# Kernel optimization log

Hardware: AMD Instinct MI355X
Metric: run time of the kernel (lower is better)

The kernel has to match this reference:

```python
import jax, jax.numpy as jnp
import numpy as np

B, S, D = 1, 2048, 2048
H, KVH, HD = 32, 8, 64  # heads, kv heads, head_dim
GROUPS = H // KVH
SCALE = HD ** -0.5


def rotate_half(x):
    x1, x2 = jnp.split(x, 2, axis=-1)
    return jnp.concatenate((-x2, x1), axis=-1)


def setup_inputs() -> dict:
    key = jax.random.key(0)
    ks = jax.random.split(key, 8)
    hidden_states = jax.random.normal(ks[0], (B, S, D), dtype=jnp.float32)
    # RoPE tables: [B, S, HD]
    inv_freq = 1.0 / (10000.0 ** (jnp.arange(0, HD, 2, dtype=jnp.float32) / HD))
    t = jnp.arange(S, dtype=jnp.float32)
    freqs = jnp.outer(t, inv_freq)                      # [S, HD/2]
    emb = jnp.concatenate((freqs, freqs), axis=-1)      # [S, HD]
    cos = jnp.cos(emb)[None]                            # [1, S, HD]
    sin = jnp.sin(emb)[None]
    std = 0.02
    wq = jax.random.normal(ks[1], (H * HD, D), dtype=jnp.float32) * std
    wk = jax.random.normal(ks[2], (KVH * HD, D), dtype=jnp.float32) * std
    wv = jax.random.normal(ks[3], (KVH * HD, D), dtype=jnp.float32) * std
    wo = jax.random.normal(ks[4], (D, H * HD), dtype=jnp.float32) * std
    return {"hidden_states": hidden_states, "cos": cos, "sin": sin,
            "wq": wq, "wk": wk, "wv": wv, "wo": wo}


def reference(hidden_states, cos, sin, wq, wk, wv, wo):
    b, s, d = hidden_states.shape
    # QKV projections (nn.Linear: x @ W.T), split into heads -> [B, H, S, HD]
    q = (hidden_states @ wq.T).reshape(b, s, H, HD).transpose(0, 2, 1, 3)
    k = (hidden_states @ wk.T).reshape(b, s, KVH, HD).transpose(0, 2, 1, 3)
    v = (hidden_states @ wv.T).reshape(b, s, KVH, HD).transpose(0, 2, 1, 3)
    # RoPE (unsqueeze_dim=1)
    c = cos[:, None, :, :]
    sn = sin[:, None, :, :]
    q = q * c + rotate_half(q) * sn
    k = k * c + rotate_half(k) * sn
    # GQA: repeat kv heads to match query heads
    k = jnp.repeat(k, GROUPS, axis=1)
    v = jnp.repeat(v, GROUPS, axis=1)
    # scaled causal softmax attention
    scores = jnp.einsum('bhqd,bhkd->bhqk', q, k) * SCALE
    causal = jnp.tril(jnp.ones((s, s), dtype=bool))
    scores = jnp.where(causal, scores, jnp.finfo(scores.dtype).min)
    probs = jax.nn.softmax(scores, axis=-1)
    attn = jnp.einsum('bhqk,bhkd->bhqd', probs, v)
    attn = attn.transpose(0, 2, 1, 3).reshape(b, s, H * HD)
    return attn @ wo.T
```

## Files before the change

kernel.cpp:

```cpp
#include <hip/hip_runtime.h>
#include <stdint.h>

#define SEQ   2048
#define DMODEL 2048
#define NQH   32
#define NKVH  8
#define HDIM  64
#define QN    (NQH*HDIM)
#define KVNN  (NKVH*HDIM)

typedef __bf16 bf16x8 __attribute__((ext_vector_type(8)));
typedef float  f32x4  __attribute__((ext_vector_type(4)));
typedef unsigned short u16;

__device__ __forceinline__ u16 f2bf(float f) {
  __bf16 h = (__bf16)f;
  return __builtin_bit_cast(u16, h);
}
__device__ __forceinline__ float bf2f(u16 b) {
  return __builtin_bit_cast(float, (uint32_t)b << 16);
}
__device__ __forceinline__ float fexp2(float x) {
#if __has_builtin(__builtin_amdgcn_exp2f)
  return __builtin_amdgcn_exp2f(x);
#else
  return __expf(0.69314718056f * x);
#endif
}
__device__ __forceinline__ bool probe_is_f32(const uint32_t* p) {
  return (p[0] & 0xFFFFu) == 0u;
}

__device__ __forceinline__ void glds16(const u16* g, void* lds) {
  __builtin_amdgcn_global_load_lds(
      (const __attribute__((address_space(1))) uint32_t*)g,
      (__attribute__((address_space(3))) uint32_t*)lds, 16, 0, 0);
}
__device__ __forceinline__ void wait_vm6() { asm volatile("s_waitcnt vmcnt(6)" ::: "memory"); }
__device__ __forceinline__ void wait_vm3() { asm volatile("s_waitcnt vmcnt(3)" ::: "memory"); }
__device__ __forceinline__ void wait_vm0() { asm volatile("s_waitcnt vmcnt(0)" ::: "memory"); }
__device__ __forceinline__ void raw_barrier() { __builtin_amdgcn_s_barrier(); }
__device__ __forceinline__ void mem_pin() { asm volatile("" ::: "memory"); }

__global__ __launch_bounds__(256)
void conv_all(const void* __restrict__ X, const void* __restrict__ cosv,
              const void* __restrict__ sinv, const void* __restrict__ wq,
              const void* __restrict__ wk, const void* __restrict__ wv,
              const void* __restrict__ wo,
              u16* __restrict__ Xc, u16* __restrict__ cosc, u16* __restrict__ sinc,
              u16* __restrict__ wqc, u16* __restrict__ wkc, u16* __restrict__ wvc,
              u16* __restrict__ woc)
{
  const bool f32in = probe_is_f32((const uint32_t*)cosv);
  const long t = (long)blockIdx.x * 256 + threadIdx.x;
  const void* src; u16* dst; long off;
  if      (t < 524288L)  { src = X;    dst = Xc;   off = t; }
  else if (t < 1048576L) { src = wq;   dst = wqc;  off = t - 524288L; }
  else if (t < 1179648L) { src = wk;   dst = wkc;  off = t - 1048576L; }
  else if (t < 1310720L) { src = wv;   dst = wvc;  off = t - 1179648L; }
  else if (t < 1835008L) { src = wo;   dst = woc;  off = t - 1310720L; }
  else if (t < 1851392L) { src = cosv; dst = cosc; off = t - 1835008L; }
  else                   { src = sinv; dst = sinc; off = t - 1851392L; }
  if (f32in) {
    const float4* s = (const float4*)src;
    float4 a = s[2*off], b = s[2*off + 1];
    union { u16 h[8]; uint4 u; } o;
    o.h[0]=f2bf(a.x); o.h[1]=f2bf(a.y); o.h[2]=f2bf(a.z); o.h[3]=f2bf(a.w);
    o.h[4]=f2bf(b.x); o.h[5]=f2bf(b.y); o.h[6]=f2bf(b.z); o.h[7]=f2bf(b.w);
    *(uint4*)(dst + off*8) = o.u;
  } else {
    *(uint4*)(dst + off*8) = ((const uint4*)src)[off];
  }
}

__global__ __launch_bounds__(256, 4)
void gemm_qkv(const u16* __restrict__ A,
              const u16* __restrict__ wq, const u16* __restrict__ wk,
              const u16* __restrict__ wv,
              u16* __restrict__ Qb, u16* __restrict__ Kb, u16* __restrict__ Vb)
{
  __shared__ __align__(16) u16 As[3][64][32];
  __shared__ __align__(16) u16 Bs[3][128][32];
  const int tid  = threadIdx.x;
  const int wave = tid >> 6;
  const int lane = tid & 63;
  const int quad = lane >> 4;
  const int l16  = lane & 15;
  const int m0 = blockIdx.y * 64;
  const int n0 = blockIdx.x * 128;
  const int wm = (wave & 1) * 32;
  const int wn = (wave >> 1) * 64;
  const int K = DMODEL;
  const int lr = lane >> 2;
  const int lc = (lane & 3) * 8;

  const u16* Bbase; u16* Cbase; int Cstride, nc0;
  if (n0 < 2048)      { Bbase = wq + (size_t)n0 * K;          Cbase = Qb; Cstride = QN;   nc0 = n0; }
  else if (n0 < 2560) { Bbase = wk + (size_t)(n0 - 2048) * K; Cbase = Kb; Cstride = KVNN; nc0 = n0 - 2048; }
  else                { Bbase = wv + (size_t)(n0 - 2560) * K; Cbase = Vb; Cstride = KVNN; nc0 = n0 - 2560; }

  f32x4 acc[2][4];
  #pragma unroll
  for (int i = 0; i < 2; i++)
    #pragma unroll
    for (int j = 0; j < 4; j++)
      acc[i][j] = (f32x4){0.f, 0.f, 0.f, 0.f};

  #define STAGE_QKV(b, k0)                                                        \
    do {                                                                          \
      glds16(A + (size_t)(m0 + 16*wave + lr) * K + (k0) + lc,                     \
             (char*)&As[b][0][0] + wave*1024);                                    \
      glds16(Bbase + (size_t)(16*wave + lr) * K + (k0) + lc,                      \
             (char*)&Bs[b][0][0] + wave*1024);                                    \
      glds16(Bbase + (size_t)(64 + 16*wave + lr) * K + (k0) + lc,                 \
             (char*)&Bs[b][0][0] + (4+wave)*1024);                                \
    } while (0)

  const int NT = K / 32;
  STAGE_QKV(0, 0);
  STAGE_QKV(1, 32);
  STAGE_QKV(2, 64);
  int cur = 0;
  for (int t = 0; t < NT; ++t) {
    if      (t < NT - 2) wait_vm6();
    else if (t == NT - 2) wait_vm3();
    else                  wait_vm0();
    raw_barrier();
    mem_pin();
    bf16x8 af[2], bfr[4];
    #pragma unroll
    for (int i = 0; i < 2; i++) af[i]  = *(const bf16x8*)&As[cur][wm + i*16 + l16][quad*8];
    #pragma unroll
    for (int j = 0; j < 4; j++) bfr[j] = *(const bf16x8*)&Bs[cur][wn + j*16 + l16][quad*8];
    #pragma unroll
    for (int i = 0; i < 2; i++)
      #pragma unroll
      for (int j = 0; j < 4; j++)
        acc[i][j] = __builtin_amdgcn_mfma_f32_16x16x32_bf16(af[i], bfr[j], acc[i][j], 0, 0, 0);
    raw_barrier();
    mem_pin();
    if (t + 3 < NT) STAGE_QKV(cur, (t + 3) * 32);
    cur = (cur == 2) ? 0 : cur + 1;
  }
  #undef STAGE_QKV

  #pragma unroll
  for (int i = 0; i < 2; i++) {
    const int rb = m0 + wm + i*16 + quad*4;
    #pragma unroll
    for (int j = 0; j < 4; j++) {
      const int col = nc0 + wn + j*16 + l16;
      #pragma unroll
      for (int r = 0; r < 4; r++)
        Cbase[(size_t)(rb + r) * Cstride + col] = f2bf(acc[i][j][r]);
    }
  }
}

__global__ __launch_bounds__(256, 4)
void gemm_nt(const u16* __restrict__ A, const u16* __restrict__ B,
             void* __restrict__ C, int M, int N, int K,
             const uint32_t* outprobe)
{
  __shared__ __align__(16) u16 As[3][64][32];
  __shared__ __align__(16) u16 Bs[3][128][32];
  const int tid  = threadIdx.x;
  const int wave = tid >> 6;
  const int lane = tid & 63;
  const int quad = lane >> 4;
  const int l16  = lane & 15;
  const int m0 = blockIdx.y * 64;
  const int n0 = blockIdx.x * 128;
  const int wm = (wave & 1) * 32;
  const int wn = (wave >> 1) * 64;
  const int lr = lane >> 2;
  const int lc = (lane & 3) * 8;

  f32x4 acc[2][4];
  #pragma unroll
  for (int i = 0; i < 2; i++)
    #pragma unroll
    for (int j = 0; j < 4; j++)
      acc[i][j] = (f32x4){0.f, 0.f, 0.f, 0.f};

  #define STAGE_NT(b, k0)                                                         \
    do {                                                                          \
      glds16(A + (size_t)(m0 + 16*wave + lr) * K + (k0) + lc,                     \
             (char*)&As[b][0][0] + wave*1024);                                    \
      glds16(B + (size_t)(n0 + 16*wave + lr) * K + (k0) + lc,                     \
             (char*)&Bs[b][0][0] + wave*1024);                                    \
      glds16(B + (size_t)(n0 + 64 + 16*wave + lr) * K + (k0) + lc,                \
             (char*)&Bs[b][0][0] + (4+wave)*1024);                                \
    } while (0)

  const int NT = K / 32;
  STAGE_NT(0, 0);
  STAGE_NT(1, 32);
  STAGE_NT(2, 64);
  int cur = 0;
  for (int t = 0; t < NT; ++t) {
    if      (t < NT - 2) wait_vm6();
    else if (t == NT - 2) wait_vm3();
    else                  wait_vm0();
    raw_barrier();
    mem_pin();
    bf16x8 af[2], bfr[4];
    #pragma unroll
    for (int i = 0; i < 2; i++) af[i]  = *(const bf16x8*)&As[cur][wm + i*16 + l16][quad*8];
    #pragma unroll
    for (int j = 0; j < 4; j++) bfr[j] = *(const bf16x8*)&Bs[cur][wn + j*16 + l16][quad*8];
    #pragma unroll
    for (int i = 0; i < 2; i++)
      #pragma unroll
      for (int j = 0; j < 4; j++)
        acc[i][j] = __builtin_amdgcn_mfma_f32_16x16x32_bf16(af[i], bfr[j], acc[i][j], 0, 0, 0);
    raw_barrier();
    mem_pin();
    if (t + 3 < NT) STAGE_NT(cur, (t + 3) * 32);
    cur = (cur == 2) ? 0 : cur + 1;
  }
  #undef STAGE_NT

  const bool f32out = (outprobe != nullptr) && probe_is_f32(outprobe);
  #pragma unroll
  for (int i = 0; i < 2; i++) {
    const int rb = m0 + wm + i*16 + quad*4;
    #pragma unroll
    for (int j = 0; j < 4; j++) {
      const int col = n0 + wn + j*16 + l16;
      if (f32out) {
        float* Cf = (float*)C;
        #pragma unroll
        for (int r = 0; r < 4; r++)
          Cf[(size_t)(rb + r) * N + col] = acc[i][j][r];
      } else {
        u16* Ch = (u16*)C;
        #pragma unroll
        for (int r = 0; r < 4; r++)
          Ch[(size_t)(rb + r) * N + col] = f2bf(acc[i][j][r]);
      }
    }
  }
}

__global__ void rope_k(u16* __restrict__ Kb,
                       const u16* __restrict__ cosb, const u16* __restrict__ sinb)
{
  const int idx = blockIdx.x * 256 + threadIdx.x;
  const int s = idx >> 8;
  const int rem = idx & 255;
  u16* base = Kb + (size_t)s * KVNN + (rem >> 5) * 64;
  const int d = rem & 31;
  const float x1 = bf2f(base[d]);
  const float x2 = bf2f(base[d + 32]);
  const float c  = bf2f(cosb[s * 64 + d]);
  const float sn = bf2f(sinb[s * 64 + d]);
  base[d]      = f2bf(x1 * c - x2 * sn);
  base[d + 32] = f2bf(x2 * c + x1 * sn);
}

__global__ __launch_bounds__(256)
void vtrans(const u16* __restrict__ Vb, u16* __restrict__ Vtg)
{
  __shared__ __align__(16) u16 T[64][72];
  const int tid = threadIdx.x;
  const int hkv = blockIdx.x & 7;
  const int s0  = (blockIdx.x >> 3) * 64;
  const int r = tid >> 3;
  const int c = (tid & 7) * 8;
  *(uint4*)&T[r][c]      = *(const uint4*)(Vb + (size_t)(s0 + r)      * KVNN + hkv*64 + c);
  *(uint4*)&T[r + 32][c] = *(const uint4*)(Vb + (size_t)(s0 + r + 32) * KVNN + hkv*64 + c);
  __syncthreads();
  #pragma unroll
  for (int dd = 0; dd < 64; dd += 32) {
    const int d = (tid >> 3) + dd;
    union { u16 h[8]; uint4 u; } o;
    #pragma unroll
    for (int j = 0; j < 8; j++) o.h[j] = T[c + j][d];
    *(uint4*)(Vtg + (size_t)(hkv*64 + d) * SEQ + s0 + c) = o.u;
  }
}

#define LOG2E 1.4426950408889634f

__global__ __launch_bounds__(256, 4)
void attn_kernel(const u16* __restrict__ Qb,
                 const u16* __restrict__ Kb,
                 const u16* __restrict__ Vtg,
                 u16* __restrict__ Ob,
                 const u16* __restrict__ cosb, const u16* __restrict__ sinb)
{
  __shared__ __align__(16) u16 Ks[64][72];
  __shared__ __align__(16) u16 Vt[64][72];
  __shared__ __align__(16) u16 Ps[4][16][72];

  const int tid  = threadIdx.x;
  const int wave = tid >> 6;
  const int lane = tid & 63;
  const int quad = lane >> 4;
  const int l16  = lane & 15;
  const int h    = blockIdx.x;
  const int qt   = 31 - blockIdx.y;
  const int hkv  = h >> 2;
  const int qrow0 = qt * 64 + wave * 16;
  const int ktmax = qt + 1;
  const int myq  = qrow0 + l16;

  bf16x8 qf[2];
  {
    const int qrow = qrow0 + l16;
    const u16* qp = Qb + (size_t)qrow * QN + h*64 + quad*8;
    union { bf16x8 v; u16 h8[8]; } lo, hi, cv, sv, olo, ohi;
    lo.v = *(const bf16x8*)qp;
    hi.v = *(const bf16x8*)(qp + 32);
    cv.v = *(const bf16x8*)(cosb + qrow*64 + quad*8);
    sv.v = *(const bf16x8*)(sinb + qrow*64 + quad*8);
    #pragma unroll
    for (int j = 0; j < 8; j++) {
      const float x1 = bf2f(lo.h8[j]), x2 = bf2f(hi.h8[j]);
      const float c = bf2f(cv.h8[j]), sn = bf2f(sv.h8[j]);
      olo.h8[j] = f2bf((x1*c - x2*sn) * 0.125f);
      ohi.h8[j] = f2bf((x2*c + x1*sn) * 0.125f);
    }
    qf[0] = olo.v;
    qf[1] = ohi.v;
  }

  f32x4 oacc[4];
  #pragma unroll
  for (int nt = 0; nt < 4; nt++) oacc[nt] = (f32x4){0.f, 0.f, 0.f, 0.f};
  float m_run = -1e30f, l_run = 0.f;

  const int sr = tid >> 3;
  const int sc = (tid & 7) * 8;

  uint4 k0, k1, v0, v1;
  {
    k0 = *(const uint4*)(Kb + (size_t)(sr)      * KVNN + hkv*64 + sc);
    k1 = *(const uint4*)(Kb + (size_t)(sr + 32) * KVNN + hkv*64 + sc);
    v0 = *(const uint4*)(Vtg + (size_t)(hkv*64 + sr)      * SEQ + sc);
    v1 = *(const uint4*)(Vtg + (size_t)(hkv*64 + sr + 32) * SEQ + sc);
  }

  for (int kt = 0; kt < ktmax; kt++) {
    const int kb = kt * 64;
    const bool diag = (kt == qt);

    __syncthreads();
    *(uint4*)&Ks[sr][sc]      = k0;
    *(uint4*)&Ks[sr + 32][sc] = k1;
    *(uint4*)&Vt[sr][sc]      = v0;
    *(uint4*)&Vt[sr + 32][sc] = v1;
    __syncthreads();

    if (kt + 1 < ktmax) {
      const int kn = kb + 64;
      k0 = *(const uint4*)(Kb + (size_t)(kn + sr)      * KVNN + hkv*64 + sc);
      k1 = *(const uint4*)(Kb + (size_t)(kn + sr + 32) * KVNN + hkv*64 + sc);
      v0 = *(const uint4*)(Vtg + (size_t)(hkv*64 + sr)      * SEQ + kn + sc);
      v1 = *(const uint4*)(Vtg + (size_t)(hkv*64 + sr + 32) * SEQ + kn + sc);
    }

    f32x4 sacc[4];
    #pragma unroll
    for (int nt = 0; nt < 4; nt++) sacc[nt] = (f32x4){0.f, 0.f, 0.f, 0.f};
    #pragma unroll
    for (int ks = 0; ks < 2; ks++)
      #pragma unroll
      for (int nt = 0; nt < 4; nt++)
        if (!diag || nt <= wave) {
          bf16x8 kf = *(const bf16x8*)&Ks[nt*16 + l16][ks*32 + quad*8];
          sacc[nt] = __builtin_amdgcn_mfma_f32_16x16x32_bf16(kf, qf[ks], sacc[nt], 0, 0, 0);
        }
    #pragma unroll
    for (int nt = 0; nt < 4; nt++)
      #pragma unroll
      for (int r = 0; r < 4; r++)
        sacc[nt][r] *= LOG2E;
    if (diag) {
      #pragma unroll
      for (int nt = 0; nt < 4; nt++)
        #pragma unroll
        for (int r = 0; r < 4; r++)
          if (kb + nt*16 + quad*4 + r > myq)
            sacc[nt][r] = -1e30f;
    }
    float mx = sacc[0][0];
    #pragma unroll
    for (int nt = 0; nt < 4; nt++)
      #pragma unroll
      for (int r = 0; r < 4; r++)
        if (nt | r) mx = fmaxf(mx, sacc[nt][r]);
    mx = fmaxf(mx, __shfl_xor(mx, 16));
    mx = fmaxf(mx, __shfl_xor(mx, 32));
    const float mnew = fmaxf(m_run, mx);
    const float alpha = fexp2(m_run - mnew);
    m_run = mnew;
    float rs = 0.f;
    #pragma unroll
    for (int nt = 0; nt < 4; nt++)
      #pragma unroll
      for (int r = 0; r < 4; r++) {
        const float p = fexp2(sacc[nt][r] - mnew);
        sacc[nt][r] = p;
        rs += p;
      }
    rs += __shfl_xor(rs, 16);
    rs += __shfl_xor(rs, 32);
    l_run = l_run * alpha + rs;
    #pragma unroll
    for (int nt = 0; nt < 4; nt++) {
      union { u16 h[4]; uint2 v; } pk;
      #pragma unroll
      for (int r = 0; r < 4; r++) pk.h[r] = f2bf(sacc[nt][r]);
      *(uint2*)&Ps[wave][l16][nt*16 + quad*4] = pk.v;
    }
    #pragma unroll
    for (int nt = 0; nt < 4; nt++)
      #pragma unroll
      for (int r = 0; r < 4; r++)
        oacc[nt][r] *= alpha;
    asm volatile("" ::: "memory");
    #pragma unroll
    for (int ks = 0; ks < 2; ks++) {
      if (diag && wave < 2 && ks == 1) continue;
      bf16x8 pf = *(const bf16x8*)&Ps[wave][l16][ks*32 + quad*8];
      #pragma unroll
      for (int nt = 0; nt < 4; nt++) {
        bf16x8 vf = *(const bf16x8*)&Vt[nt*16 + l16][ks*32 + quad*8];
        oacc[nt] = __builtin_amdgcn_mfma_f32_16x16x32_bf16(vf, pf, oacc[nt], 0, 0, 0);
      }
    }
  }

  {
    const float inv = 1.0f / l_run;
    #pragma unroll
    for (int nt = 0; nt < 4; nt++) {
      union { u16 h[4]; uint2 v; } ok;
      #pragma unroll
      for (int r = 0; r < 4; r++) ok.h[r] = f2bf(oacc[nt][r] * inv);
      *(uint2*)(Ob + (size_t)myq * QN + h*64 + nt*16 + quad*4) = ok.v;
    }
  }
}

extern "C" void kernel_launch(void* const* d_in, const int* in_sizes, int n_in,
                              void* d_out, int out_size, void* d_ws, size_t ws_size,
                              hipStream_t stream) {
  const void* X    = d_in[0];
  const void* cosr = d_in[1];
  const void* sinr = d_in[2];
  const void* wq   = d_in[3];
  const void* wk   = d_in[4];
  const void* wv   = d_in[5];
  const void* wo   = d_in[6];

  char* ws = (char*)d_ws;
  const size_t MB = 1024u * 1024u;
  u16* Xc   = (u16*)(ws);
  u16* wqc  = (u16*)(ws + 8*MB);
  u16* wkc  = (u16*)(ws + 16*MB);
  u16* wvc  = (u16*)(ws + 18*MB);
  u16* woc  = (u16*)(ws + 20*MB);
  u16* cosc = (u16*)(ws + 28*MB);
  u16* sinc = (u16*)(ws + 28*MB + 256*1024);
  u16* Qb   = (u16*)(ws + 28*MB + 512*1024);
  u16* Kb   = (u16*)(ws + 36*MB + 512*1024);
  u16* Vb   = (u16*)(ws + 38*MB + 512*1024);
  u16* Vtg  = (u16*)(ws + 40*MB + 512*1024);
  u16* Ab   = wqc;

  dim3 blk(256);
  conv_all<<<dim3(7296), blk, 0, stream>>>(X, cosr, sinr, wq, wk, wv, wo,
                                           Xc, cosc, sinc, wqc, wkc, wvc, woc);
  gemm_qkv<<<dim3(24, 32), blk, 0, stream>>>(Xc, wqc, wkc, wvc, Qb, Kb, Vb);
  rope_k<<<dim3((SEQ*NKVH*32)/256), blk, 0, stream>>>(Kb, cosc, sinc);
  vtrans<<<dim3(256), blk, 0, stream>>>(Vb, Vtg);
  attn_kernel<<<dim3(NQH, SEQ/64), blk, 0, stream>>>(Qb, Kb, Vtg, Ab, cosc, sinc);
  gemm_nt<<<dim3(16, 32), blk, 0, stream>>>(Ab, woc, d_out, SEQ, DMODEL, DMODEL,
                                            (const uint32_t*)cosr);
}
```

Baseline: 227.0 us.

## Use single-wave GEMM blocks and fuse RoPE and V transpose into QKV epilogue

Both GEMMs now run as one-wave 64x64 tiles, with each wave loading its whole tile through global-to-LDS copies and the block barriers dropped. The QKV GEMM epilogue applies RoPE to K and writes V directly in transposed layout. This removes the separate rope_k and vtrans kernel launches and their extra passes over K and V. In exchange, blocks are smaller with more in-flight loads per wave, and the V stores are scattered 8-byte writes.

```diff
diff --git a/kernel.cpp b/kernel.cpp
--- a/kernel.cpp
+++ b/kernel.cpp
@@ -36,11 +36,10 @@
       (const __attribute__((address_space(1))) uint32_t*)g,
       (__attribute__((address_space(3))) uint32_t*)lds, 16, 0, 0);
 }
-__device__ __forceinline__ void wait_vm6() { asm volatile("s_waitcnt vmcnt(6)" ::: "memory"); }
-__device__ __forceinline__ void wait_vm3() { asm volatile("s_waitcnt vmcnt(3)" ::: "memory"); }
-__device__ __forceinline__ void wait_vm0() { asm volatile("s_waitcnt vmcnt(0)" ::: "memory"); }
-__device__ __forceinline__ void raw_barrier() { __builtin_amdgcn_s_barrier(); }
-__device__ __forceinline__ void mem_pin() { asm volatile("" ::: "memory"); }
+__device__ __forceinline__ void wait_vm16() { asm volatile("s_waitcnt vmcnt(16)" ::: "memory"); }
+__device__ __forceinline__ void wait_vm8()  { asm volatile("s_waitcnt vmcnt(8)"  ::: "memory"); }
+__device__ __forceinline__ void wait_vm0()  { asm volatile("s_waitcnt vmcnt(0)"  ::: "memory"); }
+__device__ __forceinline__ void wait_lgkm0() { asm volatile("s_waitcnt lgkmcnt(0)" ::: "memory"); }
 
 __global__ __launch_bounds__(256)
 void conv_all(const void* __restrict__ X, const void* __restrict__ cosv,
@@ -73,161 +72,165 @@
   }
 }
 
-__global__ __launch_bounds__(256, 4)
+#define GEMM_LOOP(ABASE, BBASE)                                                   \
+  const int NT = K / 32;                                                          \
+  STG(0, 0); STG(1, 32); STG(2, 64);                                              \
+  int cur = 0;                                                                    \
+  for (int t = 0; t < NT; ++t) {                                                  \
+    if      (t < NT - 2) wait_vm16();                                             \
+    else if (t == NT - 2) wait_vm8();                                             \
+    else                  wait_vm0();                                             \
+    bf16x8 af[4], bfr[4];                                                         \
+    _Pragma("unroll")                                                             \
+    for (int i = 0; i < 4; i++) af[i]  = *(const bf16x8*)&As[cur][i*16 + l16][quad*8]; \
+    _Pragma("unroll")                                                             \
+    for (int j = 0; j < 4; j++) bfr[j] = *(const bf16x8*)&Bs[cur][j*16 + l16][quad*8]; \
+    _Pragma("unroll")                                                             \
+    for (int i = 0; i < 4; i++)                                                   \
+      _Pragma("unroll")                                                           \
+      for (int j = 0; j < 4; j++)                                                 \
+        acc[i][j] = __builtin_amdgcn_mfma_f32_16x16x32_bf16(af[i], bfr[j], acc[i][j], 0, 0, 0); \
+    wait_lgkm0();     \
+    if (t + 3 < NT) STG(cur, (t + 3) * 32);                                       \
+    cur = (cur == 2) ? 0 : cur + 1;                                               \
+  }
+
+__global__ __launch_bounds__(64)
 void gemm_qkv(const u16* __restrict__ A,
               const u16* __restrict__ wq, const u16* __restrict__ wk,
               const u16* __restrict__ wv,
-              u16* __restrict__ Qb, u16* __restrict__ Kb, u16* __restrict__ Vb)
+              u16* __restrict__ Qb, u16* __restrict__ Kb, u16* __restrict__ Vtg,
+              const u16* __restrict__ cosb, const u16* __restrict__ sinb)
 {
   __shared__ __align__(16) u16 As[3][64][32];
-  __shared__ __align__(16) u16 Bs[3][128][32];
-  const int tid  = threadIdx.x;
-  const int wave = tid >> 6;
-  const int lane = tid & 63;
+  __shared__ __align__(16) u16 Bs[3][64][32];
+  const int lane = threadIdx.x;
   const int quad = lane >> 4;
   const int l16  = lane & 15;
   const int m0 = blockIdx.y * 64;
-  const int n0 = blockIdx.x * 128;
-  const int wm = (wave & 1) * 32;
-  const int wn = (wave >> 1) * 64;
+  const int n0 = blockIdx.x * 64;
   const int K = DMODEL;
   const int lr = lane >> 2;
   const int lc = (lane & 3) * 8;
 
-  const u16* Bbase; u16* Cbase; int Cstride, nc0;
-  if (n0 < 2048)      { Bbase = wq + (size_t)n0 * K;          Cbase = Qb; Cstride = QN;   nc0 = n0; }
-  else if (n0 < 2560) { Bbase = wk + (size_t)(n0 - 2048) * K; Cbase = Kb; Cstride = KVNN; nc0 = n0 - 2048; }
-  else                { Bbase = wv + (size_t)(n0 - 2560) * K; Cbase = Vb; Cstride = KVNN; nc0 = n0 - 2560; }
-
-  f32x4 acc[2][4];
+  const u16* Bb; int mode, nc0;
+  if (n0 < 2048)      { Bb = wq + (size_t)n0 * K;          mode = 0; nc0 = n0; }
+  else if (n0 < 2560) { Bb = wk + (size_t)(n0 - 2048) * K; mode = 1; nc0 = n0 - 2048; }
+  else                { Bb = wv + (size_t)(n0 - 2560) * K; mode = 2; nc0 = n0 - 2560; }
+
+  f32x4 acc[4][4];
   #pragma unroll
-  for (int i = 0; i < 2; i++)
+  for (int i = 0; i < 4; i++)
     #pragma unroll
     for (int j = 0; j < 4; j++)
       acc[i][j] = (f32x4){0.f, 0.f, 0.f, 0.f};
 
-  #define STAGE_QKV(b, k0)                                                        \
+  #define STG(b, k0)                                                              \
     do {                                                                          \
-      glds16(A + (size_t)(m0 + 16*wave + lr) * K + (k0) + lc,                     \
-             (char*)&As[b][0][0] + wave*1024);                                    \
-      glds16(Bbase + (size_t)(16*wave + lr) * K + (k0) + lc,                      \
-             (char*)&Bs[b][0][0] + wave*1024);                                    \
-      glds16(Bbase + (size_t)(64 + 16*wave + lr) * K + (k0) + lc,                 \
-             (char*)&Bs[b][0][0] + (4+wave)*1024);                                \
+      _Pragma("unroll")                                                           \
+      for (int c = 0; c < 4; ++c)                                                 \
+        glds16(A  + (size_t)(m0 + 16*c + lr) * K + (k0) + lc,                     \
+               (char*)&As[b][0][0] + c*1024);                                     \
+      _Pragma("unroll")                                                           \
+      for (int c = 0; c < 4; ++c)                                                 \
+        glds16(Bb + (size_t)(16*c + lr) * K + (k0) + lc,                          \
+               (char*)&Bs[b][0][0] + c*1024);                                     \
     } while (0)
 
-  const int NT = K / 32;
-  STAGE_QKV(0, 0);
-  STAGE_QKV(1, 32);
-  STAGE_QKV(2, 64);
-  int cur = 0;
-  for (int t = 0; t < NT; ++t) {
-    if      (t < NT - 2) wait_vm6();
-    else if (t == NT - 2) wait_vm3();
-    else                  wait_vm0();
-    raw_barrier();
-    mem_pin();
-    bf16x8 af[2], bfr[4];
-    #pragma unroll
-    for (int i = 0; i < 2; i++) af[i]  = *(const bf16x8*)&As[cur][wm + i*16 + l16][quad*8];
-    #pragma unroll
-    for (int j = 0; j < 4; j++) bfr[j] = *(const bf16x8*)&Bs[cur][wn + j*16 + l16][quad*8];
-    #pragma unroll
-    for (int i = 0; i < 2; i++)
-      #pragma unroll
-      for (int j = 0; j < 4; j++)
-        acc[i][j] = __builtin_amdgcn_mfma_f32_16x16x32_bf16(af[i], bfr[j], acc[i][j], 0, 0, 0);
-    raw_barrier();
-    mem_pin();
-    if (t + 3 < NT) STAGE_QKV(cur, (t + 3) * 32);
-    cur = (cur == 2) ? 0 : cur + 1;
-  }
-  #undef STAGE_QKV
-
-  #pragma unroll
-  for (int i = 0; i < 2; i++) {
-    const int rb = m0 + wm + i*16 + quad*4;
-    #pragma unroll
-    for (int j = 0; j < 4; j++) {
-      const int col = nc0 + wn + j*16 + l16;
-      #pragma unroll
-      for (int r = 0; r < 4; r++)
-        Cbase[(size_t)(rb + r) * Cstride + col] = f2bf(acc[i][j][r]);
-    }
-  }
-}
-
-__global__ __launch_bounds__(256, 4)
+  GEMM_LOOP(A, Bb)
+  #undef STG
+
+  if (mode == 0) {
+    #pragma unroll
+    for (int i = 0; i < 4; i++) {
+      const int rb = m0 + i*16 + quad*4;
+      #pragma unroll
+      for (int j = 0; j < 4; j++) {
+        const int col = n0 + j*16 + l16;
+        #pragma unroll
+        for (int r = 0; r < 4; r++)
+          Qb[(size_t)(rb + r) * QN + col] = f2bf(acc[i][j][r]);
+      }
+    }
+  } else if (mode == 1) {
+    #pragma unroll
+    for (int i = 0; i < 4; i++) {
+      const int rb = m0 + i*16 + quad*4;
+      #pragma unroll
+      for (int j = 0; j < 2; j++) {
+        const int d = j*16 + l16;
+        #pragma unroll
+        for (int r = 0; r < 4; r++) {
+          const int s = rb + r;
+          const float c  = bf2f(cosb[s*64 + d]);
+          const float sn = bf2f(sinb[s*64 + d]);
+          const float x1 = acc[i][j][r], x2 = acc[i][j+2][r];
+          Kb[(size_t)s * KVNN + nc0 + d]      = f2bf(x1*c - x2*sn);
+          Kb[(size_t)s * KVNN + nc0 + d + 32] = f2bf(x2*c + x1*sn);
+        }
+      }
+    }
+  } else {
+    const int hkv = nc0 >> 6;
+    #pragma unroll
+    for (int i = 0; i < 4; i++) {
+      const int sbase = m0 + i*16 + quad*4;
+      #pragma unroll
+      for (int j = 0; j < 4; j++) {
+        const int d = j*16 + l16;
+        union { u16 h[4]; uint2 v; } ok;
+        #pragma unroll
+        for (int r = 0; r < 4; r++) ok.h[r] = f2bf(acc[i][j][r]);
+        *(uint2*)(Vtg + (size_t)(hkv*64 + d) * SEQ + sbase) = ok.v;
+      }
+    }
+  }
+}
+
+__global__ __launch_bounds__(64)
 void gemm_nt(const u16* __restrict__ A, const u16* __restrict__ B,
              void* __restrict__ C, int M, int N, int K,
              const uint32_t* outprobe)
 {
   __shared__ __align__(16) u16 As[3][64][32];
-  __shared__ __align__(16) u16 Bs[3][128][32];
-  const int tid  = threadIdx.x;
-  const int wave = tid >> 6;
-  const int lane = tid & 63;
+  __shared__ __align__(16) u16 Bs[3][64][32];
+  const int lane = threadIdx.x;
   const int quad = lane >> 4;
   const int l16  = lane & 15;
   const int m0 = blockIdx.y * 64;
-  const int n0 = blockIdx.x * 128;
-  const int wm = (wave & 1) * 32;
-  const int wn = (wave >> 1) * 64;
+  const int n0 = blockIdx.x * 64;
   const int lr = lane >> 2;
   const int lc = (lane & 3) * 8;
 
-  f32x4 acc[2][4];
+  f32x4 acc[4][4];
   #pragma unroll
-  for (int i = 0; i < 2; i++)
+  for (int i = 0; i < 4; i++)
     #pragma unroll
     for (int j = 0; j < 4; j++)
       acc[i][j] = (f32x4){0.f, 0.f, 0.f, 0.f};
 
-  #define STAGE_NT(b, k0)                                                         \
+  #define STG(b, k0)                                                              \
     do {                                                                          \
-      glds16(A + (size_t)(m0 + 16*wave + lr) * K + (k0) + lc,                     \
-             (char*)&As[b][0][0] + wave*1024);                                    \
-      glds16(B + (size_t)(n0 + 16*wave + lr) * K + (k0) + lc,                     \
-             (char*)&Bs[b][0][0] + wave*1024);                                    \
-      glds16(B + (size_t)(n0 + 64 + 16*wave + lr) * K + (k0) + lc,                \
-             (char*)&Bs[b][0][0] + (4+wave)*1024);                                \
+      _Pragma("unroll")                                                           \
+      for (int c = 0; c < 4; ++c)                                                 \
+        glds16(A + (size_t)(m0 + 16*c + lr) * K + (k0) + lc,                      \
+               (char*)&As[b][0][0] + c*1024);                                     \
+      _Pragma("unroll")                                                           \
+      for (int c = 0; c < 4; ++c)                                                 \
+        glds16(B + (size_t)(n0 + 16*c + lr) * K + (k0) + lc,                      \
+               (char*)&Bs[b][0][0] + c*1024);                                     \
     } while (0)
 
-  const int NT = K / 32;
-  STAGE_NT(0, 0);
-  STAGE_NT(1, 32);
-  STAGE_NT(2, 64);
-  int cur = 0;
-  for (int t = 0; t < NT; ++t) {
-    if      (t < NT - 2) wait_vm6();
-    else if (t == NT - 2) wait_vm3();
-    else                  wait_vm0();
-    raw_barrier();
-    mem_pin();
-    bf16x8 af[2], bfr[4];
-    #pragma unroll
-    for (int i = 0; i < 2; i++) af[i]  = *(const bf16x8*)&As[cur][wm + i*16 + l16][quad*8];
-    #pragma unroll
-    for (int j = 0; j < 4; j++) bfr[j] = *(const bf16x8*)&Bs[cur][wn + j*16 + l16][quad*8];
-    #pragma unroll
-    for (int i = 0; i < 2; i++)
-      #pragma unroll
-      for (int j = 0; j < 4; j++)
-        acc[i][j] = __builtin_amdgcn_mfma_f32_16x16x32_bf16(af[i], bfr[j], acc[i][j], 0, 0, 0);
-    raw_barrier();
-    mem_pin();
-    if (t + 3 < NT) STAGE_NT(cur, (t + 3) * 32);
-    cur = (cur == 2) ? 0 : cur + 1;
-  }
-  #undef STAGE_NT
+  GEMM_LOOP(A, B)
+  #undef STG
 
   const bool f32out = (outprobe != nullptr) && probe_is_f32(outprobe);
   #pragma unroll
-  for (int i = 0; i < 2; i++) {
-    const int rb = m0 + wm + i*16 + quad*4;
+  for (int i = 0; i < 4; i++) {
+    const int rb = m0 + i*16 + quad*4;
     #pragma unroll
     for (int j = 0; j < 4; j++) {
-      const int col = n0 + wn + j*16 + l16;
+      const int col = n0 + j*16 + l16;
       if (f32out) {
         float* Cf = (float*)C;
         #pragma unroll
@@ -240,44 +243,6 @@
           Ch[(size_t)(rb + r) * N + col] = f2bf(acc[i][j][r]);
       }
     }
-  }
-}
-
-__global__ void rope_k(u16* __restrict__ Kb,
-                       const u16* __restrict__ cosb, const u16* __restrict__ sinb)
-{
-  const int idx = blockIdx.x * 256 + threadIdx.x;
-  const int s = idx >> 8;
-  const int rem = idx & 255;
-  u16* base = Kb + (size_t)s * KVNN + (rem >> 5) * 64;
-  const int d = rem & 31;
-  const float x1 = bf2f(base[d]);
-  const float x2 = bf2f(base[d + 32]);
-  const float c  = bf2f(cosb[s * 64 + d]);
-  const float sn = bf2f(sinb[s * 64 + d]);
-  base[d]      = f2bf(x1 * c - x2 * sn);
-  base[d + 32] = f2bf(x2 * c + x1 * sn);
-}
-
-__global__ __launch_bounds__(256)
-void vtrans(const u16* __restrict__ Vb, u16* __restrict__ Vtg)
-{
-  __shared__ __align__(16) u16 T[64][72];
-  const int tid = threadIdx.x;
-  const int hkv = blockIdx.x & 7;
-  const int s0  = (blockIdx.x >> 3) * 64;
-  const int r = tid >> 3;
-  const int c = (tid & 7) * 8;
-  *(uint4*)&T[r][c]      = *(const uint4*)(Vb + (size_t)(s0 + r)      * KVNN + hkv*64 + c);
-  *(uint4*)&T[r + 32][c] = *(const uint4*)(Vb + (size_t)(s0 + r + 32) * KVNN + hkv*64 + c);
-  __syncthreads();
-  #pragma unroll
-  for (int dd = 0; dd < 64; dd += 32) {
-    const int d = (tid >> 3) + dd;
-    union { u16 h[8]; uint4 u; } o;
-    #pragma unroll
-    for (int j = 0; j < 8; j++) o.h[j] = T[c + j][d];
-    *(uint4*)(Vtg + (size_t)(hkv*64 + d) * SEQ + s0 + c) = o.u;
   }
 }
 
@@ -467,17 +432,15 @@
   u16* sinc = (u16*)(ws + 28*MB + 256*1024);
   u16* Qb   = (u16*)(ws + 28*MB + 512*1024);
   u16* Kb   = (u16*)(ws + 36*MB + 512*1024);
-  u16* Vb   = (u16*)(ws + 38*MB + 512*1024);
   u16* Vtg  = (u16*)(ws + 40*MB + 512*1024);
   u16* Ab   = wqc;
 
-  dim3 blk(256);
-  conv_all<<<dim3(7296), blk, 0, stream>>>(X, cosr, sinr, wq, wk, wv, wo,
-                                           Xc, cosc, sinc, wqc, wkc, wvc, woc);
-  gemm_qkv<<<dim3(24, 32), blk, 0, stream>>>(Xc, wqc, wkc, wvc, Qb, Kb, Vb);
-  rope_k<<<dim3((SEQ*NKVH*32)/256), blk, 0, stream>>>(Kb, cosc, sinc);
-  vtrans<<<dim3(256), blk, 0, stream>>>(Vb, Vtg);
-  attn_kernel<<<dim3(NQH, SEQ/64), blk, 0, stream>>>(Qb, Kb, Vtg, Ab, cosc, sinc);
-  gemm_nt<<<dim3(16, 32), blk, 0, stream>>>(Ab, woc, d_out, SEQ, DMODEL, DMODEL,
+  dim3 b64(64), b256(256);
+  conv_all<<<dim3(7296), b256, 0, stream>>>(X, cosr, sinr, wq, wk, wv, wo,
+                                            Xc, cosc, sinc, wqc, wkc, wvc, woc);
+  gemm_qkv<<<dim3(48, 32), b64, 0, stream>>>(Xc, wqc, wkc, wvc, Qb, Kb, Vtg,
+                                             cosc, sinc);
+  attn_kernel<<<dim3(NQH, SEQ/64), b256, 0, stream>>>(Qb, Kb, Vtg, Ab, cosc, sinc);
+  gemm_nt<<<dim3(32, 32), b64, 0, stream>>>(Ab, woc, d_out, SEQ, DMODEL, DMODEL,
                                             (const uint32_t*)cosr);
 }
```

After: 248.8 us. 9.6% more time.

## Fuse K RoPE and V transpose into QKV GEMM epilogue

Applied to the files above, without the earlier changes.

The QKV projection GEMM epilogue now applies rotary embedding to K tiles directly from accumulators and writes V already transposed into the head-major layout. This removes the separate rope_k and vtrans kernels, their launches and the extra global round trips through Kb and Vb. The cost is a heavier, branchy epilogue, and the transposed V stores are 8-byte strided writes rather than coalesced rows.

```diff
diff --git a/kernel.cpp b/kernel.cpp
--- a/kernel.cpp
+++ b/kernel.cpp
@@ -77,7 +77,8 @@
 void gemm_qkv(const u16* __restrict__ A,
               const u16* __restrict__ wq, const u16* __restrict__ wk,
               const u16* __restrict__ wv,
-              u16* __restrict__ Qb, u16* __restrict__ Kb, u16* __restrict__ Vb)
+              u16* __restrict__ Qb, u16* __restrict__ Kb, u16* __restrict__ Vtg,
+              const u16* __restrict__ cosb, const u16* __restrict__ sinb)
 {
   __shared__ __align__(16) u16 As[3][64][32];
   __shared__ __align__(16) u16 Bs[3][128][32];
@@ -94,10 +95,10 @@
   const int lr = lane >> 2;
   const int lc = (lane & 3) * 8;
 
-  const u16* Bbase; u16* Cbase; int Cstride, nc0;
-  if (n0 < 2048)      { Bbase = wq + (size_t)n0 * K;          Cbase = Qb; Cstride = QN;   nc0 = n0; }
-  else if (n0 < 2560) { Bbase = wk + (size_t)(n0 - 2048) * K; Cbase = Kb; Cstride = KVNN; nc0 = n0 - 2048; }
-  else                { Bbase = wv + (size_t)(n0 - 2560) * K; Cbase = Vb; Cstride = KVNN; nc0 = n0 - 2560; }
+  const u16* Bb; int mode, nc0;
+  if (n0 < 2048)      { Bb = wq + (size_t)n0 * K;          mode = 0; nc0 = n0; }
+  else if (n0 < 2560) { Bb = wk + (size_t)(n0 - 2048) * K; mode = 1; nc0 = n0 - 2048; }
+  else                { Bb = wv + (size_t)(n0 - 2560) * K; mode = 2; nc0 = n0 - 2560; }
 
   f32x4 acc[2][4];
   #pragma unroll
@@ -110,9 +111,9 @@
     do {                                                                          \
       glds16(A + (size_t)(m0 + 16*wave + lr) * K + (k0) + lc,                     \
              (char*)&As[b][0][0] + wave*1024);                                    \
-      glds16(Bbase + (size_t)(16*wave + lr) * K + (k0) + lc,                      \
+      glds16(Bb + (size_t)(16*wave + lr) * K + (k0) + lc,                         \
              (char*)&Bs[b][0][0] + wave*1024);                                    \
-      glds16(Bbase + (size_t)(64 + 16*wave + lr) * K + (k0) + lc,                 \
+      glds16(Bb + (size_t)(64 + 16*wave + lr) * K + (k0) + lc,                    \
              (char*)&Bs[b][0][0] + (4+wave)*1024);                                \
     } while (0)
 
@@ -144,15 +145,50 @@
   }
   #undef STAGE_QKV
 
-  #pragma unroll
-  for (int i = 0; i < 2; i++) {
-    const int rb = m0 + wm + i*16 + quad*4;
-    #pragma unroll
-    for (int j = 0; j < 4; j++) {
-      const int col = nc0 + wn + j*16 + l16;
-      #pragma unroll
-      for (int r = 0; r < 4; r++)
-        Cbase[(size_t)(rb + r) * Cstride + col] = f2bf(acc[i][j][r]);
+  if (mode == 0) {
+    #pragma unroll
+    for (int i = 0; i < 2; i++) {
+      const int rb = m0 + wm + i*16 + quad*4;
+      #pragma unroll
+      for (int j = 0; j < 4; j++) {
+        const int col = nc0 + wn + j*16 + l16;
+        #pragma unroll
+        for (int r = 0; r < 4; r++)
+          Qb[(size_t)(rb + r) * QN + col] = f2bf(acc[i][j][r]);
+      }
+    }
+  } else if (mode == 1) {
+    const int hc = nc0 + wn;
+    #pragma unroll
+    for (int i = 0; i < 2; i++) {
+      const int rb = m0 + wm + i*16 + quad*4;
+      #pragma unroll
+      for (int j = 0; j < 2; j++) {
+        const int d = j*16 + l16;
+        #pragma unroll
+        for (int r = 0; r < 4; r++) {
+          const int s = rb + r;
+          const float c  = bf2f(cosb[s*64 + d]);
+          const float sn = bf2f(sinb[s*64 + d]);
+          const float x1 = acc[i][j][r], x2 = acc[i][j+2][r];
+          Kb[(size_t)s * KVNN + hc + d]      = f2bf(x1*c - x2*sn);
+          Kb[(size_t)s * KVNN + hc + d + 32] = f2bf(x2*c + x1*sn);
+        }
+      }
+    }
+  } else {
+    const int hkv = (nc0 + wn) >> 6;
+    #pragma unroll
+    for (int i = 0; i < 2; i++) {
+      const int sbase = m0 + wm + i*16 + quad*4;
+      #pragma unroll
+      for (int j = 0; j < 4; j++) {
+        const int d = j*16 + l16;
+        union { u16 h[4]; uint2 v; } ok;
+        #pragma unroll
+        for (int r = 0; r < 4; r++) ok.h[r] = f2bf(acc[i][j][r]);
+        *(uint2*)(Vtg + (size_t)(hkv*64 + d) * SEQ + sbase) = ok.v;
+      }
     }
   }
 }
@@ -243,44 +279,6 @@
   }
 }
 
-__global__ void rope_k(u16* __restrict__ Kb,
-                       const u16* __restrict__ cosb, const u16* __restrict__ sinb)
-{
-  const int idx = blockIdx.x * 256 + threadIdx.x;
-  const int s = idx >> 8;
-  const int rem = idx & 255;
-  u16* base = Kb + (size_t)s * KVNN + (rem >> 5) * 64;
-  const int d = rem & 31;
-  const float x1 = bf2f(base[d]);
-  const float x2 = bf2f(base[d + 32]);
-  const float c  = bf2f(cosb[s * 64 + d]);
-  const float sn = bf2f(sinb[s * 64 + d]);
-  base[d]      = f2bf(x1 * c - x2 * sn);
-  base[d + 32] = f2bf(x2 * c + x1 * sn);
-}
-
-__global__ __launch_bounds__(256)
-void vtrans(const u16* __restrict__ Vb, u16* __restrict__ Vtg)
-{
-  __shared__ __align__(16) u16 T[64][72];
-  const int tid = threadIdx.x;
-  const int hkv = blockIdx.x & 7;
-  const int s0  = (blockIdx.x >> 3) * 64;
-  const int r = tid >> 3;
-  const int c = (tid & 7) * 8;
-  *(uint4*)&T[r][c]      = *(const uint4*)(Vb + (size_t)(s0 + r)      * KVNN + hkv*64 + c);
-  *(uint4*)&T[r + 32][c] = *(const uint4*)(Vb + (size_t)(s0 + r + 32) * KVNN + hkv*64 + c);
-  __syncthreads();
-  #pragma unroll
-  for (int dd = 0; dd < 64; dd += 32) {
-    const int d = (tid >> 3) + dd;
-    union { u16 h[8]; uint4 u; } o;
-    #pragma unroll
-    for (int j = 0; j < 8; j++) o.h[j] = T[c + j][d];
-    *(uint4*)(Vtg + (size_t)(hkv*64 + d) * SEQ + s0 + c) = o.u;
-  }
-}
-
 #define LOG2E 1.4426950408889634f
 
 __global__ __launch_bounds__(256, 4)
@@ -467,17 +465,15 @@
   u16* sinc = (u16*)(ws + 28*MB + 256*1024);
   u16* Qb   = (u16*)(ws + 28*MB + 512*1024);
   u16* Kb   = (u16*)(ws + 36*MB + 512*1024);
-  u16* Vb   = (u16*)(ws + 38*MB + 512*1024);
   u16* Vtg  = (u16*)(ws + 40*MB + 512*1024);
   u16* Ab   = wqc;
 
-  dim3 blk(256);
-  conv_all<<<dim3(7296), blk, 0, stream>>>(X, cosr, sinr, wq, wk, wv, wo,
-                                           Xc, cosc, sinc, wqc, wkc, wvc, woc);
-  gemm_qkv<<<dim3(24, 32), blk, 0, stream>>>(Xc, wqc, wkc, wvc, Qb, Kb, Vb);
-  rope_k<<<dim3((SEQ*NKVH*32)/256), blk, 0, stream>>>(Kb, cosc, sinc);
-  vtrans<<<dim3(256), blk, 0, stream>>>(Vb, Vtg);
-  attn_kernel<<<dim3(NQH, SEQ/64), blk, 0, stream>>>(Qb, Kb, Vtg, Ab, cosc, sinc);
-  gemm_nt<<<dim3(16, 32), blk, 0, stream>>>(Ab, woc, d_out, SEQ, DMODEL, DMODEL,
-                                            (const uint32_t*)cosr);
-}
+  dim3 b256(256);
+  conv_all<<<dim3(7296), b256, 0, stream>>>(X, cosr, sinr, wq, wk, wv, wo,
+                                            Xc, cosc, sinc, wqc, wkc, wvc, woc);
+  gemm_qkv<<<dim3(24, 32), b256, 0, stream>>>(Xc, wqc, wkc, wvc, Qb, Kb, Vtg,
+                                              cosc, sinc);
+  attn_kernel<<<dim3(NQH, SEQ/64), b256, 0, stream>>>(Qb, Kb, Vtg, Ab, cosc, sinc);
+  gemm_nt<<<dim3(16, 32), b256, 0, stream>>>(Ab, woc, d_out, SEQ, DMODEL, DMODEL,
+                                             (const uint32_t*)cosr);
+}
```

After: 224.4 us. Within noise of the previous version (-1.2%).
